# Kernel optimization log

Hardware: AMD Instinct MI355X
Metric: run time of the kernel (lower is better)

Reference implementation:

```python
import jax, jax.numpy as jnp
import numpy as np

ALPHA = 0.1  # cfg.model.mmd.attention_temperature
EPS = 1e-12


def _l2norm(x, axis=-1):
    return x / jnp.sqrt(jnp.sum(x * x, axis=axis, keepdims=True) + EPS)


def setup_inputs() -> dict:
    key = jax.random.key(0)
    k1, k2, k3, k4 = jax.random.split(key, 4)
    b, ng, nl, nf, c = 8, 5, 75, 196, 640
    return {
        "global_f": jax.random.normal(k1, (b, ng, c), dtype=jnp.float32),
        "local_f": jax.random.normal(k2, (b, nl, nf, c), dtype=jnp.float32),
        "Wq": jax.random.normal(k3, (c, c), dtype=jnp.float32) / np.sqrt(c),
        "Wk": jax.random.normal(k4, (c, c), dtype=jnp.float32) / np.sqrt(c),
    }


def reference(global_f, local_f, Wq, Wk):
    # AttentiveMMDPrompt.compute_attn_weight with dim=1, num_groups=1.
    b, ng, c = global_f.shape
    _, nl, nf, _ = local_f.shape
    # q/k projections (nn.Linear, no bias): x @ W^T
    g = jnp.einsum('bgc,dc->bgd', global_f, Wq)          # [b, ng, c]
    l = jnp.einsum('blfc,dc->blfd', local_f, Wk)         # [b, nl, nf, c]
    # centering: subtract joint per-episode mean feature over all tokens
    tot = g.sum(axis=1) + l.sum(axis=(1, 2))             # [b, c]
    mean = tot / (ng + nl * nf)
    g = g - mean[:, None, :]
    l = l - mean[:, None, None, :]
    # l2 normalize feature vectors
    g = _l2norm(g)
    l = _l2norm(l)
    # score: local_f @ global_f -> [b, nl, ng, nf]
    scores = jnp.einsum('blfc,bgc->blgf', l, g) / ALPHA
    attn = jax.nn.softmax(scores, axis=-1)               # softmax over nf
    return attn[..., None]                               # [b, nl, ng, nf, 1]
```

## Files before the change

### kernel.cpp

```cpp
#include <hip/hip_runtime.h>
#include <math.h>

namespace {
constexpr int kB = 8, kNG = 5, kNL = 75, kNF = 196, kC = 640;
constexpr int kNTokL = kNL * kNF;
constexpr int kNTot = kNG + kNTokL;
constexpr float kEps = 1e-12f;
constexpr float kInvAlpha = 10.0f;
constexpr int kKC = 20;
constexpr int kTiles = 230;
constexpr int kNT = 5;
}

typedef __attribute__((ext_vector_type(8))) short short8;
typedef __attribute__((ext_vector_type(4))) short short4v;
typedef __attribute__((ext_vector_type(4))) float floatx4;

union S8U { short8 v; ushort u[8]; };
union S4U { short4v v; ushort u[4]; };

__device__ __forceinline__ void bsplit(float x, ushort& h, ushort& l) {
  union { float f; uint u; } a; a.f = x;
  uint uh = (a.u + 0x7FFFu + ((a.u >> 16) & 1u)) >> 16;
  h = (ushort)uh;
  union { uint u; float f; } bb; bb.u = uh << 16;
  float r = x - bb.f;
  union { float f; uint u; } c; c.f = r;
  l = (ushort)((c.u + 0x7FFFu + ((c.u >> 16) & 1u)) >> 16);
}

#define MFMA_BF16(a, b, c) __builtin_amdgcn_mfma_f32_16x16x32_bf16(a, b, c, 0, 0, 0)

__device__ __forceinline__ void bar_lds() {
  asm volatile("s_waitcnt lgkmcnt(0)\n\ts_barrier" ::: "memory");
}

__global__ void k_sumcvt(const float* __restrict__ lf, float* __restrict__ s_l,
                         const float* __restrict__ Wk, ushort* __restrict__ Wh,
                         ushort* __restrict__ Wl) {
  const int tid = threadIdx.x;
  if (blockIdx.x < 1840) {
    const int b = blockIdx.x & 7, slice = blockIdx.x >> 3;
    const int c4 = tid % 160, h = tid / 160;
    const int t0 = slice * 64 + h * 32;
    const int nrow = min(32, kNTokL - t0);
    const float* p = lf + ((size_t)b * kNTokL + t0) * kC + c4 * 4;
    float4 acc = {0.f, 0.f, 0.f, 0.f};
#pragma unroll 4
    for (int i = 0; i < nrow; ++i) {
      const float4 v = *(const float4*)(p + (size_t)i * kC);
      acc.x += v.x; acc.y += v.y; acc.z += v.z; acc.w += v.w;
    }
    __shared__ float4 sred[160];
    if (h == 1) sred[c4] = acc;
    __syncthreads();
    if (h == 0) {
      const float4 o = sred[c4];
      acc.x += o.x; acc.y += o.y; acc.z += o.z; acc.w += o.w;
      float* dst = &s_l[b * kC + c4 * 4];
      atomicAdd(dst + 0, acc.x);
      atomicAdd(dst + 1, acc.y);
      atomicAdd(dst + 2, acc.z);
      atomicAdd(dst + 3, acc.w);
    }
  } else {
    const int wv = (blockIdx.x - 1840) * 5 + (tid >> 6);
    const int lane = tid & 63;
    const int kc = wv % kKC, dt = wv / kKC;
    const int fm = lane & 15, quad = lane >> 4;
    const float* p = Wk + (size_t)(dt * 16 + fm) * kC + kc * 32 + quad * 8;
    float4 a = *(const float4*)p;
    float4 c = *(const float4*)(p + 4);
    S8U h, l;
    bsplit(a.x, h.u[0], l.u[0]); bsplit(a.y, h.u[1], l.u[1]);
    bsplit(a.z, h.u[2], l.u[2]); bsplit(a.w, h.u[3], l.u[3]);
    bsplit(c.x, h.u[4], l.u[4]); bsplit(c.y, h.u[5], l.u[5]);
    bsplit(c.z, h.u[6], l.u[6]); bsplit(c.w, h.u[7], l.u[7]);
    const size_t off = ((size_t)kc * 40 + dt) * 512 + (size_t)lane * 8;
    *(short8*)(Wh + off) = h.v;
    *(short8*)(Wl + off) = l.v;
  }
}

__global__ void k_proj_mean(const float* __restrict__ Wq, const float* __restrict__ Wk,
                            const float* __restrict__ gf, const float* __restrict__ s_l,
                            float* __restrict__ m, float* __restrict__ gc) {
  const int wid = blockIdx.x * 4 + (threadIdx.x >> 6);
  const int lane = threadIdx.x & 63;
  const int b = wid / kC, d = wid % kC;
  float ak = 0.f, ag[kNG] = {0.f, 0.f, 0.f, 0.f, 0.f};
  for (int c = lane; c < kC; c += 64) {
    const float wq = Wq[d * kC + c];
    const float wk = Wk[d * kC + c];
    ak += wk * s_l[b * kC + c];
#pragma unroll
    for (int g = 0; g < kNG; ++g) ag[g] += wq * gf[(b * kNG + g) * kC + c];
  }
#pragma unroll
  for (int off = 32; off > 0; off >>= 1) {
    ak += __shfl_xor(ak, off);
#pragma unroll
    for (int g = 0; g < kNG; ++g) ag[g] += __shfl_xor(ag[g], off);
  }
  if (lane == 0) {
    float aq = 0.f;
#pragma unroll
    for (int g = 0; g < kNG; ++g) aq += ag[g];
    const float mv = (aq + ak) / (float)kNTot;
    m[b * kC + d] = mv;
#pragma unroll
    for (int g = 0; g < kNG; ++g) gc[(b * kNG + g) * kC + d] = ag[g] - mv;
  }
}

__global__ void k_norm_g(const float* __restrict__ gc, float* __restrict__ gn) {
  const int row = blockIdx.x;
  __shared__ float red[256];
  float a = 0.f;
  for (int d = threadIdx.x; d < kC; d += 256) {
    const float v = gc[row * kC + d];
    a += v * v;
  }
  red[threadIdx.x] = a;
  __syncthreads();
  for (int s = 128; s > 0; s >>= 1) {
    if (threadIdx.x < s) red[threadIdx.x] += red[threadIdx.x + s];
    __syncthreads();
  }
  const float rs = 1.0f / sqrtf(red[0] + kEps);
  for (int d = threadIdx.x; d < kC; d += 256) gn[row * kC + d] = gc[row * kC + d] * rs;
}

__global__ __launch_bounds__(1024, 4) void k_big(
    const float* __restrict__ lf, const ushort* __restrict__ Wh,
    const ushort* __restrict__ Wl, const float* __restrict__ m,
    const float* __restrict__ gn, float* __restrict__ scores) {
  __shared__ ushort smem[16384];
  float* red = (float*)smem;

  const int tid = threadIdx.x;
  const int wv = tid >> 6, lane = tid & 63;
  const int wn = wv >> 1, th2 = (wv & 1) * 2;
  const int fm = lane & 15, quad = lane >> 4;
  const int b = blockIdx.x & 7, tile = blockIdx.x >> 3;
  const int tok0 = tile * 64;

  const int sr = tid >> 4, sq = tid & 15;
  int strow = tok0 + sr;
  if (strow >= kNTokL) strow = kNTokL - 1;
  const float* xrow = lf + ((size_t)b * kNTokL + strow) * kC + sq * 4;
  const int kq = sq & 7;
  const int aoff = ((sq >> 3) * 4 + (sr >> 4)) * 512 + ((kq >> 1) * 16 + (sr & 15)) * 8 + (kq & 1) * 4;

  floatx4 acc[2][kNT];
#pragma unroll
  for (int i = 0; i < 2; ++i)
#pragma unroll
    for (int j = 0; j < kNT; ++j) acc[i][j] = (floatx4){0.f, 0.f, 0.f, 0.f};

#define STAGE(XV, BUF)                                        \
  {                                                           \
    S4U _h, _l;                                               \
    bsplit((XV).x, _h.u[0], _l.u[0]);                         \
    bsplit((XV).y, _h.u[1], _l.u[1]);                         \
    bsplit((XV).z, _h.u[2], _l.u[2]);                         \
    bsplit((XV).w, _h.u[3], _l.u[3]);                         \
    *(short4v*)(smem + (BUF) + aoff) = _h.v;                  \
    *(short4v*)(smem + (BUF) + 4096 + aoff) = _l.v;           \
  }

#define LOADB(KCI)                                                            \
  {                                                                           \
    const size_t _o = ((size_t)(KCI) * 40 + wn * 5) * 512 + (size_t)lane * 8; \
    _Pragma("unroll") for (int nt = 0; nt < kNT; ++nt) {                      \
      BH[nt] = *(const short8*)(Wh + _o + nt * 512);                          \
      BL[nt] = *(const short8*)(Wl + _o + nt * 512);                          \
    }                                                                         \
  }

#define READA(BUF, CI)                                                        \
  {                                                                           \
    _Pragma("unroll") for (int mt = 0; mt < 2; ++mt) {                        \
      const int _ba = (BUF) + ((CI) * 4 + th2 + mt) * 512 + lane * 8;         \
      ah[mt] = *(const short8*)(smem + _ba);                                  \
      al[mt] = *(const short8*)(smem + _ba + 4096);                           \
    }                                                                         \
  }

#define DOMFMA3                                                               \
  {                                                                           \
    _Pragma("unroll") for (int nt = 0; nt < kNT; ++nt)                        \
        _Pragma("unroll") for (int mt = 0; mt < 2; ++mt)                      \
            acc[mt][nt] = MFMA_BF16(ah[mt], BH[nt], acc[mt][nt]);             \
    _Pragma("unroll") for (int nt = 0; nt < kNT; ++nt)                        \
        _Pragma("unroll") for (int mt = 0; mt < 2; ++mt)                      \
            acc[mt][nt] = MFMA_BF16(al[mt], BH[nt], acc[mt][nt]);             \
    _Pragma("unroll") for (int nt = 0; nt < kNT; ++nt)                        \
        _Pragma("unroll") for (int mt = 0; mt < 2; ++mt)                      \
            acc[mt][nt] = MFMA_BF16(ah[mt], BL[nt], acc[mt][nt]);             \
  }

  short8 ah[2], al[2];
  short8 BH[kNT], BL[kNT];
  float4 xcur = *(const float4*)xrow;
  STAGE(xcur, 0);
  float4 xnext = *(const float4*)(xrow + 64);
  for (int t = 0; t < 10; ++t) {
    const int buff = (t & 1) * 8192;
    bar_lds();
    if (t < 9) STAGE(xnext, ((t + 1) & 1) * 8192);
    if (t < 8) xnext = *(const float4*)(xrow + (t + 2) * 64);
    LOADB(2 * t);
    READA(buff, 0);
    DOMFMA3;
    LOADB(2 * t + 1);
    READA(buff, 1);
    DOMFMA3;
  }

  float mv[kNT], gvv[5][kNT];
#pragma unroll
  for (int nt = 0; nt < kNT; ++nt) {
    const int d = wn * 80 + nt * 16 + fm;
    mv[nt] = m[b * kC + d];
#pragma unroll
    for (int g = 0; g < 5; ++g) gvv[g][nt] = gn[(b * kNG + g) * kC + d];
  }

  bar_lds();
#pragma unroll
  for (int mt = 0; mt < 2; ++mt)
#pragma unroll
    for (int reg = 0; reg < 4; ++reg) {
      float part[6] = {0.f, 0.f, 0.f, 0.f, 0.f, 0.f};
#pragma unroll
      for (int nt = 0; nt < kNT; ++nt) {
        const float yc = acc[mt][nt][reg] - mv[nt];
        part[0] += yc * yc;
#pragma unroll
        for (int g = 0; g < 5; ++g) part[1 + g] += yc * gvv[g][nt];
      }
#pragma unroll
      for (int off = 1; off < 16; off <<= 1)
#pragma unroll
        for (int v = 0; v < 6; ++v) part[v] += __shfl_xor(part[v], off);
      if (fm == 0) {
        const int row = mt * 16 + quad * 4 + reg;
#pragma unroll
        for (int v = 0; v < 6; ++v) red[((size_t)wv * 32 + row) * 6 + v] = part[v];
      }
    }
  bar_lds();
  if (tid < 64) {
    const int tok = tok0 + tid;
    if (tok < kNTokL) {
      const int tht = tid >> 5, row = tid & 31;
      float s[6] = {0.f, 0.f, 0.f, 0.f, 0.f, 0.f};
#pragma unroll
      for (int w = 0; w < 8; ++w)
#pragma unroll
        for (int v = 0; v < 6; ++v) s[v] += red[((size_t)(w * 2 + tht) * 32 + row) * 6 + v];
      const float rs = (1.0f / sqrtf(s[0] + kEps)) * kInvAlpha;
      const size_t t = (size_t)b * kNTokL + tok;
#pragma unroll
      for (int g = 0; g < 5; ++g)
        scores[(size_t)g * (kB * kNTokL) + t] = s[1 + g] * rs;
    }
  }
#undef STAGE
#undef LOADB
#undef READA
#undef DOMFMA3
}

__global__ void k_softmax(const float* __restrict__ scores, float* __restrict__ out) {
  const int wid = blockIdx.x * 4 + (threadIdx.x >> 6);
  const int lane = threadIdx.x & 63;
  const int b = wid / (kNL * kNG);
  const int rem = wid % (kNL * kNG);
  const int l = rem / kNG, g = rem % kNG;
  float sv[4];
  float mx = -1e30f;
#pragma unroll
  for (int u = 0; u < 4; ++u) {
    const int f = lane + 64 * u;
    if (f < kNF) {
      const size_t t = (size_t)b * kNTokL + (size_t)l * kNF + f;
      sv[u] = scores[(size_t)g * (kB * kNTokL) + t];
      mx = fmaxf(mx, sv[u]);
    } else {
      sv[u] = 0.f;
    }
  }
#pragma unroll
  for (int off = 32; off > 0; off >>= 1) mx = fmaxf(mx, __shfl_xor(mx, off));
  float se = 0.f;
#pragma unroll
  for (int u = 0; u < 4; ++u) {
    const int f = lane + 64 * u;
    const float e = (f < kNF) ? expf(sv[u] - mx) : 0.f;
    sv[u] = e;
    se += e;
  }
#pragma unroll
  for (int off = 32; off > 0; off >>= 1) se += __shfl_xor(se, off);
  const float inv = 1.0f / se;
#pragma unroll
  for (int u = 0; u < 4; ++u) {
    const int f = lane + 64 * u;
    if (f < kNF) out[((size_t)(b * kNL + l) * kNG + g) * kNF + f] = sv[u] * inv;
  }
}


extern "C" void kernel_launch(void* const* d_in, const int* in_sizes, int n_in,
                              void* d_out, int out_size, void* d_ws, size_t ws_size,
                              hipStream_t stream) {
  (void)in_sizes; (void)n_in; (void)out_size; (void)ws_size;
  const float* gf = (const float*)d_in[0];
  const float* lf = (const float*)d_in[1];
  const float* Wq = (const float*)d_in[2];
  const float* Wk = (const float*)d_in[3];
  float* ws = (float*)d_ws;
  float* out = (float*)d_out;

  float* s_l    = ws;
  float* m      = ws + 5120;
  float* gc     = ws + 10240;
  float* gn     = ws + 35840;
  float* scores = ws + 61440;
  ushort* Wh    = (ushort*)(ws + 649440);
  ushort* Wl    = (ushort*)(ws + 854240);

  hipMemsetAsync(s_l, 0, (size_t)5120 * 4, stream);

  k_sumcvt<<<2000, 320, 0, stream>>>(lf, s_l, Wk, Wh, Wl);
  k_proj_mean<<<(kB * kC) / 4, 256, 0, stream>>>(Wq, Wk, gf, s_l, m, gc);
  k_norm_g<<<kB * kNG, 256, 0, stream>>>(gc, gn);
  k_big<<<kTiles * kB, 1024, 0, stream>>>(lf, Wh, Wl, m, gn, scores);
  k_softmax<<<750, 256, 0, stream>>>(scores, out);
}
```

Before: 834.3 us.

## Enlarge k_big token tile to 128 rows with 8 waves each covering full M

New measurement: 746.6 us. -10.5%, faster.

```diff
diff --git a/kernel.cpp b/kernel.cpp
--- a/kernel.cpp
+++ b/kernel.cpp
@@ -8,16 +8,14 @@
 constexpr float kEps = 1e-12f;
 constexpr float kInvAlpha = 10.0f;
 constexpr int kKC = 20;
-constexpr int kTiles = 230;
+constexpr int kTiles = 115;
 constexpr int kNT = 5;
 }
 
 typedef __attribute__((ext_vector_type(8))) short short8;
-typedef __attribute__((ext_vector_type(4))) short short4v;
 typedef __attribute__((ext_vector_type(4))) float floatx4;
 
 union S8U { short8 v; ushort u[8]; };
-union S4U { short4v v; ushort u[4]; };
 
 __device__ __forceinline__ void bsplit(float x, ushort& h, ushort& l) {
   union { float f; uint u; } a; a.f = x;
@@ -131,91 +129,92 @@
   for (int d = threadIdx.x; d < kC; d += 256) gn[row * kC + d] = gc[row * kC + d] * rs;
 }
 
-__global__ __launch_bounds__(1024, 4) void k_big(
+__global__ __launch_bounds__(512, 2) void k_big(
     const float* __restrict__ lf, const ushort* __restrict__ Wh,
     const ushort* __restrict__ Wl, const float* __restrict__ m,
     const float* __restrict__ gn, float* __restrict__ scores) {
-  __shared__ ushort smem[16384];
+  __shared__ ushort smem[32768];
   float* red = (float*)smem;
 
   const int tid = threadIdx.x;
-  const int wv = tid >> 6, lane = tid & 63;
-  const int wn = wv >> 1, th2 = (wv & 1) * 2;
+  const int wn = tid >> 6, lane = tid & 63;
   const int fm = lane & 15, quad = lane >> 4;
   const int b = blockIdx.x & 7, tile = blockIdx.x >> 3;
-  const int tok0 = tile * 64;
-
-  const int sr = tid >> 4, sq = tid & 15;
+  const int tok0 = tile * 128;
+
+  const int sr = tid >> 2, sq = tid & 3;
   int strow = tok0 + sr;
   if (strow >= kNTokL) strow = kNTokL - 1;
-  const float* xrow = lf + ((size_t)b * kNTokL + strow) * kC + sq * 4;
-  const int kq = sq & 7;
-  const int aoff = ((sq >> 3) * 4 + (sr >> 4)) * 512 + ((kq >> 1) * 16 + (sr & 15)) * 8 + (kq & 1) * 4;
-
-  floatx4 acc[2][kNT];
-#pragma unroll
-  for (int i = 0; i < 2; ++i)
+  const float* xrow = lf + ((size_t)b * kNTokL + strow) * kC + sq * 8;
+  const int aoff = ((sr >> 4) << 9) + ((sq * 16 + (sr & 15)) << 3);
+
+  floatx4 acc[8][kNT];
+#pragma unroll
+  for (int i = 0; i < 8; ++i)
 #pragma unroll
     for (int j = 0; j < kNT; ++j) acc[i][j] = (floatx4){0.f, 0.f, 0.f, 0.f};
 
-#define STAGE(XV, BUF)                                        \
-  {                                                           \
-    S4U _h, _l;                                               \
-    bsplit((XV).x, _h.u[0], _l.u[0]);                         \
-    bsplit((XV).y, _h.u[1], _l.u[1]);                         \
-    bsplit((XV).z, _h.u[2], _l.u[2]);                         \
-    bsplit((XV).w, _h.u[3], _l.u[3]);                         \
-    *(short4v*)(smem + (BUF) + aoff) = _h.v;                  \
-    *(short4v*)(smem + (BUF) + 4096 + aoff) = _l.v;           \
-  }
-
-#define LOADB(KCI)                                                            \
+#define STAGEKC(F0, F1, BUFOFF)                                        \
+  {                                                                    \
+    S8U _h, _l;                                                        \
+    bsplit((F0).x, _h.u[0], _l.u[0]); bsplit((F0).y, _h.u[1], _l.u[1]);\
+    bsplit((F0).z, _h.u[2], _l.u[2]); bsplit((F0).w, _h.u[3], _l.u[3]);\
+    bsplit((F1).x, _h.u[4], _l.u[4]); bsplit((F1).y, _h.u[5], _l.u[5]);\
+    bsplit((F1).z, _h.u[6], _l.u[6]); bsplit((F1).w, _h.u[7], _l.u[7]);\
+    *(short8*)(smem + (BUFOFF) + aoff) = _h.v;                         \
+    *(short8*)(smem + (BUFOFF) + 8192 + aoff) = _l.v;                  \
+  }
+
+#define DOSUB(BUF, KCL, KCI)                                                  \
   {                                                                           \
-    const size_t _o = ((size_t)(KCI) * 40 + wn * 5) * 512 + (size_t)lane * 8; \
+    const ushort* _bh = Wh + ((size_t)(KCI) * 40 + wn * 5) * 512 + (size_t)lane * 8; \
+    const ushort* _bl = Wl + ((size_t)(KCI) * 40 + wn * 5) * 512 + (size_t)lane * 8; \
+    short8 BH[kNT], BL[kNT];                                                  \
     _Pragma("unroll") for (int nt = 0; nt < kNT; ++nt) {                      \
-      BH[nt] = *(const short8*)(Wh + _o + nt * 512);                          \
-      BL[nt] = *(const short8*)(Wl + _o + nt * 512);                          \
+      BH[nt] = *(const short8*)(_bh + nt * 512);                              \
+      BL[nt] = *(const short8*)(_bl + nt * 512);                              \
     }                                                                         \
-  }
-
-#define READA(BUF, CI)                                                        \
-  {                                                                           \
-    _Pragma("unroll") for (int mt = 0; mt < 2; ++mt) {                        \
-      const int _ba = (BUF) + ((CI) * 4 + th2 + mt) * 512 + lane * 8;         \
-      ah[mt] = *(const short8*)(smem + _ba);                                  \
-      al[mt] = *(const short8*)(smem + _ba + 4096);                           \
+    _Pragma("unroll") for (int mt = 0; mt < 8; ++mt) {                        \
+      const int _ba = (BUF) + (KCL) * 4096 + mt * 512 + lane * 8;             \
+      const short8 ah = *(const short8*)(smem + _ba);                         \
+      const short8 al = *(const short8*)(smem + _ba + 8192);                  \
+      _Pragma("unroll") for (int nt = 0; nt < kNT; ++nt)                      \
+          acc[mt][nt] = MFMA_BF16(ah, BH[nt], acc[mt][nt]);                   \
+      _Pragma("unroll") for (int nt = 0; nt < kNT; ++nt)                      \
+          acc[mt][nt] = MFMA_BF16(al, BH[nt], acc[mt][nt]);                   \
+      _Pragma("unroll") for (int nt = 0; nt < kNT; ++nt)                      \
+          acc[mt][nt] = MFMA_BF16(ah, BL[nt], acc[mt][nt]);                   \
     }                                                                         \
   }
 
-#define DOMFMA3                                                               \
-  {                                                                           \
-    _Pragma("unroll") for (int nt = 0; nt < kNT; ++nt)                        \
-        _Pragma("unroll") for (int mt = 0; mt < 2; ++mt)                      \
-            acc[mt][nt] = MFMA_BF16(ah[mt], BH[nt], acc[mt][nt]);             \
-    _Pragma("unroll") for (int nt = 0; nt < kNT; ++nt)                        \
-        _Pragma("unroll") for (int mt = 0; mt < 2; ++mt)                      \
-            acc[mt][nt] = MFMA_BF16(al[mt], BH[nt], acc[mt][nt]);             \
-    _Pragma("unroll") for (int nt = 0; nt < kNT; ++nt)                        \
-        _Pragma("unroll") for (int mt = 0; mt < 2; ++mt)                      \
-            acc[mt][nt] = MFMA_BF16(ah[mt], BL[nt], acc[mt][nt]);             \
-  }
-
-  short8 ah[2], al[2];
-  short8 BH[kNT], BL[kNT];
-  float4 xcur = *(const float4*)xrow;
-  STAGE(xcur, 0);
-  float4 xnext = *(const float4*)(xrow + 64);
+  float4 x0 = *(const float4*)(xrow);
+  float4 x1 = *(const float4*)(xrow + 4);
+  float4 x2 = *(const float4*)(xrow + 32);
+  float4 x3 = *(const float4*)(xrow + 36);
+  STAGEKC(x0, x1, 0);
+  STAGEKC(x2, x3, 4096);
+  x0 = *(const float4*)(xrow + 64);
+  x1 = *(const float4*)(xrow + 68);
+  x2 = *(const float4*)(xrow + 96);
+  x3 = *(const float4*)(xrow + 100);
+
   for (int t = 0; t < 10; ++t) {
-    const int buff = (t & 1) * 8192;
+    const int buf = (t & 1) * 16384;
+    const int obuf = buf ^ 16384;
     bar_lds();
-    if (t < 9) STAGE(xnext, ((t + 1) & 1) * 8192);
-    if (t < 8) xnext = *(const float4*)(xrow + (t + 2) * 64);
-    LOADB(2 * t);
-    READA(buff, 0);
-    DOMFMA3;
-    LOADB(2 * t + 1);
-    READA(buff, 1);
-    DOMFMA3;
+    if (t < 9) {
+      STAGEKC(x0, x1, obuf);
+      STAGEKC(x2, x3, obuf + 4096);
+    }
+    if (t < 8) {
+      const float* xs = xrow + (t + 2) * 64;
+      x0 = *(const float4*)(xs);
+      x1 = *(const float4*)(xs + 4);
+      x2 = *(const float4*)(xs + 32);
+      x3 = *(const float4*)(xs + 36);
+    }
+    DOSUB(buf, 0, 2 * t);
+    DOSUB(buf, 1, 2 * t + 1);
   }
 
   float mv[kNT], gvv[5][kNT];
@@ -229,7 +228,7 @@
 
   bar_lds();
 #pragma unroll
-  for (int mt = 0; mt < 2; ++mt)
+  for (int mt = 0; mt < 8; ++mt)
 #pragma unroll
     for (int reg = 0; reg < 4; ++reg) {
       float part[6] = {0.f, 0.f, 0.f, 0.f, 0.f, 0.f};
@@ -247,19 +246,18 @@
       if (fm == 0) {
         const int row = mt * 16 + quad * 4 + reg;
 #pragma unroll
-        for (int v = 0; v < 6; ++v) red[((size_t)wv * 32 + row) * 6 + v] = part[v];
+        for (int v = 0; v < 6; ++v) red[((size_t)wn * 128 + row) * 6 + v] = part[v];
       }
     }
   bar_lds();
-  if (tid < 64) {
+  if (tid < 128) {
     const int tok = tok0 + tid;
     if (tok < kNTokL) {
-      const int tht = tid >> 5, row = tid & 31;
       float s[6] = {0.f, 0.f, 0.f, 0.f, 0.f, 0.f};
 #pragma unroll
       for (int w = 0; w < 8; ++w)
 #pragma unroll
-        for (int v = 0; v < 6; ++v) s[v] += red[((size_t)(w * 2 + tht) * 32 + row) * 6 + v];
+        for (int v = 0; v < 6; ++v) s[v] += red[((size_t)w * 128 + tid) * 6 + v];
       const float rs = (1.0f / sqrtf(s[0] + kEps)) * kInvAlpha;
       const size_t t = (size_t)b * kNTokL + tok;
 #pragma unroll
@@ -267,10 +265,8 @@
         scores[(size_t)g * (kB * kNTokL) + t] = s[1 + g] * rs;
     }
   }
-#undef STAGE
-#undef LOADB
-#undef READA
-#undef DOMFMA3
+#undef STAGEKC
+#undef DOSUB
 }
 
 __global__ void k_softmax(const float* __restrict__ scores, float* __restrict__ out) {
@@ -337,6 +333,6 @@
   k_sumcvt<<<2000, 320, 0, stream>>>(lf, s_l, Wk, Wh, Wl);
   k_proj_mean<<<(kB * kC) / 4, 256, 0, stream>>>(Wq, Wk, gf, s_l, m, gc);
   k_norm_g<<<kB * kNG, 256, 0, stream>>>(gc, gn);
-  k_big<<<kTiles * kB, 1024, 0, stream>>>(lf, Wh, Wl, m, gn, scores);
+  k_big<<<kTiles * kB, 512, 0, stream>>>(lf, Wh, Wl, m, gn, scores);
   k_softmax<<<750, 256, 0, stream>>>(scores, out);
 }
```
